# Kernel optimization log

Hardware: AMD Instinct MI355X
Metric: run time of the kernel (lower is better)

## Reference

```python
import jax, jax.numpy as jnp
import numpy as np

N = 100000      # active input voxels (== output voxels, stride=1)
K = 27          # kernel volume: 3**3 hypercube offsets
M = 50000       # active in/out pairs per kernel offset
CIN = 64
COUT = 64


def setup_inputs() -> dict:
    key = jax.random.key(0)
    k1, k2, k3, k4 = jax.random.split(key, 4)
    std = (2.0 / CIN / K) ** 0.5
    x = jax.random.normal(k1, (N, CIN), dtype=jnp.float32)
    kernel = jax.random.normal(k2, (K, CIN, COUT), dtype=jnp.float32) * std
    bias = jnp.zeros((1, COUT), dtype=jnp.float32)
    in_map = jax.random.randint(k3, (K, M), 0, N, dtype=jnp.int64)
    out_map = jax.random.randint(k4, (K, M), 0, N, dtype=jnp.int64)
    return {"x": x, "kernel": kernel, "bias": bias,
            "in_map": in_map, "out_map": out_map}


def reference(x, kernel, bias, in_map, out_map):
    # Sparse voxel convolution: per kernel-offset gather -> matmul -> scatter-add.
    gathered = x[in_map]                                   # [K, M, Cin]
    prod = jnp.einsum('kmc,kcd->kmd', gathered, kernel)    # [K, M, Cout]
    out = jnp.zeros((N, COUT), dtype=x.dtype)
    out = out.at[out_map.reshape(-1)].add(prod.reshape(-1, COUT))
    out = out + bias                                       # bias is [1, Cout]
    return out
```

## Files before the change

kernel.cpp:

```cpp
#include <hip/hip_runtime.h>
#include <hip/hip_fp16.h>

#define N_VOX 100000
#define KVOL 27
#define MPAIR 50000
#define CIN 64
#define COUT 64
#define TPW 4
#define NTILES 3125
#define GRIDX 196

typedef __attribute__((ext_vector_type(8))) short bf16x8;
typedef __attribute__((ext_vector_type(4))) float f32x4;
typedef __attribute__((ext_vector_type(4))) unsigned short u16x4;

__device__ inline unsigned short f2bf(float f) {
    union { float f; unsigned u; } v; v.f = f;
    return (unsigned short)((v.u + 0x7FFFu + ((v.u >> 16) & 1u)) >> 16);
}

__global__ void spconv_zero_ws(__half2* __restrict__ ws, int n2) {
    int i = blockIdx.x * blockDim.x + threadIdx.x;
    if (i < n2) ws[i] = __float2half2_rn(0.f);
}

__global__ void spconv_x_to_bf16(const float* __restrict__ x,
                                 unsigned short* __restrict__ xbf, int n4) {
    int i = blockIdx.x * blockDim.x + threadIdx.x;
    if (i >= n4) return;
    f32x4 v = ((const f32x4*)x)[i];
    u16x4 o; o.x = f2bf(v.x); o.y = f2bf(v.y); o.z = f2bf(v.z); o.w = f2bf(v.w);
    ((u16x4*)xbf)[i] = o;
}

__global__ void spconv_finalize(const __half2* __restrict__ ws,
                                const float* __restrict__ bias,
                                float* __restrict__ out, int n2) {
    int i = blockIdx.x * blockDim.x + threadIdx.x;
    if (i >= n2) return;
    float2 v = __half22float2(ws[i]);
    int c2 = (i & (COUT / 2 - 1)) * 2;
    float2 o; o.x = v.x + bias[c2]; o.y = v.y + bias[c2 + 1];
    ((float2*)out)[i] = o;
}

__global__ __launch_bounds__(256) void spconv_mlp_f16ws(
    const unsigned short* __restrict__ xbf,
    const float* __restrict__ kern,
    const int*   __restrict__ in_map,
    const int*   __restrict__ out_map,
    __half2*     __restrict__ ws)
{
    const int lane = threadIdx.x & 63;
    const int wave = threadIdx.x >> 6;
    const int k    = blockIdx.y;
    const int g    = lane >> 4;
    const int r16  = lane & 15;
    const int p    = r16 & 1;

    const int tile0 = (blockIdx.x * 4 + wave) * TPW;
    const int base0 = k * MPAIR;

    int inrow[TPW];
    #pragma unroll
    for (int t = 0; t < TPW; ++t) {
        int tl = tile0 + t; tl = tl < NTILES ? tl : NTILES - 1;
        inrow[t] = in_map[base0 + tl * 16 + r16];
    }

    bf16x8 afr[TPW][2];
    #pragma unroll
    for (int t = 0; t < TPW; ++t) {
        const unsigned short* xp = xbf + (size_t)inrow[t] * CIN + g * 8;
        afr[t][0] = *(const bf16x8*)(xp);
        afr[t][1] = *(const bf16x8*)(xp + 32);
    }

    int orow[TPW][4];
    #pragma unroll
    for (int t = 0; t < TPW; ++t) {
        int tl = tile0 + t; tl = tl < NTILES ? tl : NTILES - 1;
        #pragma unroll
        for (int r = 0; r < 4; ++r)
            orow[t][r] = out_map[base0 + tl * 16 + g * 4 + r];
    }

    bf16x8 bfrag[2][4];
    {
        const float* wp = kern + (size_t)k * CIN * COUT;
        #pragma unroll
        for (int s = 0; s < 2; ++s)
            #pragma unroll
            for (int q = 0; q < 4; ++q) {
                const float* pq = wp + (s * 32 + g * 8) * COUT + q * 16 + r16;
                bf16x8 f;
                #pragma unroll
                for (int j = 0; j < 8; ++j) f[j] = (short)f2bf(pq[j * COUT]);
                bfrag[s][q] = f;
            }
    }

    #pragma unroll
    for (int t = 0; t < TPW; ++t) {
        if (tile0 + t < NTILES) {
            f32x4 acc[4] = {{0.f,0.f,0.f,0.f},{0.f,0.f,0.f,0.f},
                            {0.f,0.f,0.f,0.f},{0.f,0.f,0.f,0.f}};
            #pragma unroll
            for (int q = 0; q < 4; ++q) {
                acc[q] = __builtin_amdgcn_mfma_f32_16x16x32_bf16(afr[t][0], bfrag[0][q], acc[q], 0, 0, 0);
                acc[q] = __builtin_amdgcn_mfma_f32_16x16x32_bf16(afr[t][1], bfrag[1][q], acc[q], 0, 0, 0);
            }
            #pragma unroll
            for (int r = 0; r < 4; ++r) {
                float pv[4];
                #pragma unroll
                for (int q = 0; q < 4; ++q) pv[q] = __shfl_xor(acc[q][r], 1);
                __half2* wrow = ws + (size_t)orow[t][r] * (COUT / 2);
                #pragma unroll
                for (int q = 0; q < 2; ++q) {
                    int tt = 2 * p + q;
                    float lo = p ? pv[tt] : acc[tt][r];
                    float hi = p ? acc[tt][r] : pv[tt];
                    int col = tt * 16 + r16 - p;
                    unsafeAtomicAdd(wrow + (col >> 1), __floats2half2_rn(lo, hi));
                }
            }
        }
    }
}

__global__ void spconv_init_bias(const float* __restrict__ bias,
                                 float* __restrict__ out, int total) {
    int i = blockIdx.x * blockDim.x + threadIdx.x;
    if (i < total) out[i] = bias[i & (COUT - 1)];
}

__global__ __launch_bounds__(256) void spconv_mfma_mlp(
    const unsigned short* __restrict__ xbf,
    const float* __restrict__ kern,
    const int*   __restrict__ in_map,
    const int*   __restrict__ out_map,
    float*       __restrict__ out)
{
    const int lane = threadIdx.x & 63;
    const int wave = threadIdx.x >> 6;
    const int k    = blockIdx.y;
    const int g    = lane >> 4;
    const int r16  = lane & 15;

    const int tile0 = (blockIdx.x * 4 + wave) * TPW;
    const int base0 = k * MPAIR;

    int inrow[TPW];
    #pragma unroll
    for (int t = 0; t < TPW; ++t) {
        int tl = tile0 + t; tl = tl < NTILES ? tl : NTILES - 1;
        inrow[t] = in_map[base0 + tl * 16 + r16];
    }
    bf16x8 afr[TPW][2];
    #pragma unroll
    for (int t = 0; t < TPW; ++t) {
        const unsigned short* xp = xbf + (size_t)inrow[t] * CIN + g * 8;
        afr[t][0] = *(const bf16x8*)(xp);
        afr[t][1] = *(const bf16x8*)(xp + 32);
    }
    int orow[TPW][4];
    #pragma unroll
    for (int t = 0; t < TPW; ++t) {
        int tl = tile0 + t; tl = tl < NTILES ? tl : NTILES - 1;
        #pragma unroll
        for (int r = 0; r < 4; ++r)
            orow[t][r] = out_map[base0 + tl * 16 + g * 4 + r];
    }
    bf16x8 bfrag[2][4];
    {
        const float* wp = kern + (size_t)k * CIN * COUT;
        #pragma unroll
        for (int s = 0; s < 2; ++s)
            #pragma unroll
            for (int q = 0; q < 4; ++q) {
                const float* pq = wp + (s * 32 + g * 8) * COUT + q * 16 + r16;
                bf16x8 f;
                #pragma unroll
                for (int j = 0; j < 8; ++j) f[j] = (short)f2bf(pq[j * COUT]);
                bfrag[s][q] = f;
            }
    }
    #pragma unroll
    for (int t = 0; t < TPW; ++t) {
        if (tile0 + t < NTILES) {
            f32x4 acc[4] = {{0.f,0.f,0.f,0.f},{0.f,0.f,0.f,0.f},
                            {0.f,0.f,0.f,0.f},{0.f,0.f,0.f,0.f}};
            #pragma unroll
            for (int q = 0; q < 4; ++q) {
                acc[q] = __builtin_amdgcn_mfma_f32_16x16x32_bf16(afr[t][0], bfrag[0][q], acc[q], 0, 0, 0);
                acc[q] = __builtin_amdgcn_mfma_f32_16x16x32_bf16(afr[t][1], bfrag[1][q], acc[q], 0, 0, 0);
            }
            #pragma unroll
            for (int r = 0; r < 4; ++r) {
                float* op = out + (size_t)orow[t][r] * COUT + r16;
                #pragma unroll
                for (int q = 0; q < 4; ++q)
                    atomicAdd(op + q * 16, acc[q][r]);
            }
        }
    }
}

extern "C" void kernel_launch(void* const* d_in, const int* in_sizes, int n_in,
                              void* d_out, int out_size, void* d_ws, size_t ws_size,
                              hipStream_t stream) {
    const float* x       = (const float*)d_in[0];
    const float* kern    = (const float*)d_in[1];
    const float* bias    = (const float*)d_in[2];
    const int*   in_map  = (const int*)d_in[3];
    const int*   out_map = (const int*)d_in[4];
    float*       out     = (float*)d_out;

    const size_t xbf_bytes = (size_t)N_VOX * CIN * sizeof(unsigned short);
    const size_t ws_bytes  = (size_t)N_VOX * COUT * sizeof(__half);
    int n4 = N_VOX * CIN / 4;
    int n2 = N_VOX * COUT / 2;
    dim3 grid(GRIDX, KVOL);

    if (ws_size >= xbf_bytes + ws_bytes) {
        unsigned short* xbf = (unsigned short*)d_ws;
        __half2* ws = (__half2*)((char*)d_ws + xbf_bytes);
        spconv_x_to_bf16<<<(n4 + 255) / 256, 256, 0, stream>>>(x, xbf, n4);
        spconv_zero_ws<<<(n2 + 255) / 256, 256, 0, stream>>>(ws, n2);
        spconv_mlp_f16ws<<<grid, 256, 0, stream>>>(xbf, kern, in_map, out_map, ws);
        spconv_finalize<<<(n2 + 255) / 256, 256, 0, stream>>>(ws, bias, out, n2);
    } else {
        unsigned short* xbf = (unsigned short*)d_ws;
        int total = N_VOX * COUT;
        spconv_init_bias<<<(total + 255) / 256, 256, 0, stream>>>(bias, out, total);
        spconv_x_to_bf16<<<(n4 + 255) / 256, 256, 0, stream>>>(x, xbf, n4);
        spconv_mfma_mlp<<<grid, 256, 0, stream>>>(xbf, kern, in_map, out_map, out);
    }
}
```

Measured before the change: 372.2 us.

## Replace atomic scatter-add with counting-sort slots and per-output segmented reduction

Removes the scatter-add atomics from the main kernel. A histogram over out_map assigns each pair a slot, and a single-block scan builds row pointers. The MFMA kernel then writes each product row as bf16 into its own slot with plain stores. A final kernel sums each output row's slots in fp32 and adds the bias. This trades about 43M half2 atomics for a much larger workspace and extra launches: histogram atomics, a serial single-block scan, and writing and reading back about 170MB of slots. The new path runs only when the workspace is big enough.

```diff
diff --git a/kernel.cpp b/kernel.cpp
--- a/kernel.cpp
+++ b/kernel.cpp
@@ -9,6 +9,7 @@
 #define TPW 4
 #define NTILES 3125
 #define GRIDX 196
+#define NPAIR (KVOL * MPAIR)
 
 typedef __attribute__((ext_vector_type(8))) short bf16x8;
 typedef __attribute__((ext_vector_type(4))) float f32x4;
@@ -18,11 +19,10 @@
     union { float f; unsigned u; } v; v.f = f;
     return (unsigned short)((v.u + 0x7FFFu + ((v.u >> 16) & 1u)) >> 16);
 }
-
-__global__ void spconv_zero_ws(__half2* __restrict__ ws, int n2) {
-    int i = blockIdx.x * blockDim.x + threadIdx.x;
-    if (i < n2) ws[i] = __float2half2_rn(0.f);
-}
+__device__ inline float bf2f(unsigned short u) {
+    union { unsigned u; float f; } v; v.u = (unsigned)u << 16; return v.f;
+}
+
 
 __global__ void spconv_x_to_bf16(const float* __restrict__ x,
                                  unsigned short* __restrict__ xbf, int n4) {
@@ -31,6 +31,147 @@
     f32x4 v = ((const f32x4*)x)[i];
     u16x4 o; o.x = f2bf(v.x); o.y = f2bf(v.y); o.z = f2bf(v.z); o.w = f2bf(v.w);
     ((u16x4*)xbf)[i] = o;
+}
+
+__global__ void spconv_zero_i32(int* __restrict__ p, int n) {
+    int i = blockIdx.x * blockDim.x + threadIdx.x;
+    if (i < n) p[i] = 0;
+}
+
+
+__global__ void spconv_hist_alloc(const int* __restrict__ out_map,
+                                  int* __restrict__ cnt,
+                                  int* __restrict__ off, int tot) {
+    int i = blockIdx.x * blockDim.x + threadIdx.x;
+    if (i < tot) off[i] = atomicAdd(&cnt[out_map[i]], 1);
+}
+
+__global__ __launch_bounds__(1024) void spconv_scan(const int* __restrict__ cnt,
+                                                    int* __restrict__ rowptr) {
+    __shared__ int part[1024];
+    const int T = 1024, C = (N_VOX + T - 1) / T;
+    int tid = threadIdx.x;
+    int base = tid * C, s = 0;
+    for (int j = 0; j < C; ++j) { int idx = base + j; if (idx < N_VOX) s += cnt[idx]; }
+    part[tid] = s;
+    __syncthreads();
+    for (int d = 1; d < T; d <<= 1) {
+        int v = (tid >= d) ? part[tid - d] : 0;
+        __syncthreads();
+        part[tid] += v;
+        __syncthreads();
+    }
+    int run = (tid == 0) ? 0 : part[tid - 1];
+    for (int j = 0; j < C; ++j) {
+        int idx = base + j;
+        if (idx < N_VOX) { rowptr[idx] = run; run += cnt[idx]; }
+    }
+    if (tid == T - 1) rowptr[N_VOX] = run;
+}
+
+__global__ __launch_bounds__(256) void spconv_phaseA(
+    const unsigned short* __restrict__ xbf,
+    const float* __restrict__ kern,
+    const int*   __restrict__ in_map,
+    const int*   __restrict__ out_map,
+    const int*   __restrict__ off,
+    const int*   __restrict__ rowptr,
+    unsigned short* __restrict__ slots)
+{
+    const int lane = threadIdx.x & 63;
+    const int wave = threadIdx.x >> 6;
+    const int k    = blockIdx.y;
+    const int g    = lane >> 4;
+    const int r16  = lane & 15;
+    const int p    = r16 & 1;
+
+    const int tile0 = (blockIdx.x * 4 + wave) * TPW;
+    const int base0 = k * MPAIR;
+
+    int inrow[TPW];
+    #pragma unroll
+    for (int t = 0; t < TPW; ++t) {
+        int tl = tile0 + t; tl = tl < NTILES ? tl : NTILES - 1;
+        inrow[t] = in_map[base0 + tl * 16 + r16];
+    }
+    bf16x8 afr[TPW][2];
+    #pragma unroll
+    for (int t = 0; t < TPW; ++t) {
+        const unsigned short* xp = xbf + (size_t)inrow[t] * CIN + g * 8;
+        afr[t][0] = *(const bf16x8*)(xp);
+        afr[t][1] = *(const bf16x8*)(xp + 32);
+    }
+    int sid_mine[TPW];
+    #pragma unroll
+    for (int t = 0; t < TPW; ++t) {
+        int tl = tile0 + t; tl = tl < NTILES ? tl : NTILES - 1;
+        int ip = base0 + tl * 16 + g * 4 + (r16 & 3);
+        sid_mine[t] = rowptr[out_map[ip]] + off[ip];
+    }
+    bf16x8 bfrag[2][4];
+    {
+        const float* wp = kern + (size_t)k * CIN * COUT;
+        #pragma unroll
+        for (int s = 0; s < 2; ++s)
+            #pragma unroll
+            for (int q = 0; q < 4; ++q) {
+                const float* pq = wp + (s * 32 + g * 8) * COUT + q * 16 + r16;
+                bf16x8 f;
+                #pragma unroll
+                for (int j = 0; j < 8; ++j) f[j] = (short)f2bf(pq[j * COUT]);
+                bfrag[s][q] = f;
+            }
+    }
+    #pragma unroll
+    for (int t = 0; t < TPW; ++t) {
+        if (tile0 + t < NTILES) {
+            f32x4 acc[4] = {{0.f,0.f,0.f,0.f},{0.f,0.f,0.f,0.f},
+                            {0.f,0.f,0.f,0.f},{0.f,0.f,0.f,0.f}};
+            #pragma unroll
+            for (int q = 0; q < 4; ++q) {
+                acc[q] = __builtin_amdgcn_mfma_f32_16x16x32_bf16(afr[t][0], bfrag[0][q], acc[q], 0, 0, 0);
+                acc[q] = __builtin_amdgcn_mfma_f32_16x16x32_bf16(afr[t][1], bfrag[1][q], acc[q], 0, 0, 0);
+            }
+            #pragma unroll
+            for (int r = 0; r < 4; ++r) {
+                int sid = __shfl(sid_mine[t], (lane & 48) + r);
+                float pv[4];
+                #pragma unroll
+                for (int q = 0; q < 4; ++q) pv[q] = __shfl_xor(acc[q][r], 1);
+                unsigned* srow = (unsigned*)(slots + (size_t)sid * COUT);
+                #pragma unroll
+                for (int q2 = 0; q2 < 2; ++q2) {
+                    int tt = 2 * p + q2;
+                    float lo = p ? pv[tt] : acc[tt][r];
+                    float hi = p ? acc[tt][r] : pv[tt];
+                    unsigned pk = (unsigned)f2bf(lo) | ((unsigned)f2bf(hi) << 16);
+                    int col = tt * 16 + r16 - p;
+                    srow[col >> 1] = pk;
+                }
+            }
+        }
+    }
+}
+
+__global__ __launch_bounds__(256) void spconv_phaseB(
+    const unsigned short* __restrict__ slots,
+    const int*   __restrict__ rowptr,
+    const float* __restrict__ bias,
+    float*       __restrict__ out)
+{
+    int w = threadIdx.x >> 6, l = threadIdx.x & 63;
+    int o = blockIdx.x * 4 + w;
+    int s0 = rowptr[o], s1 = rowptr[o + 1];
+    float acc = 0.f;
+    for (int s = s0; s < s1; ++s)
+        acc += bf2f(slots[(size_t)s * COUT + l]);
+    out[(size_t)o * COUT + l] = acc + bias[l];
+}
+
+
+__global__ void spconv_zero_ws(__half2* __restrict__ ws, int n2) {
+    int i = blockIdx.x * blockDim.x + threadIdx.x;
+    if (i < n2) ws[i] = __float2half2_rn(0.f);
 }
 
 __global__ void spconv_finalize(const __half2* __restrict__ ws,
@@ -67,7 +208,6 @@
         int tl = tile0 + t; tl = tl < NTILES ? tl : NTILES - 1;
         inrow[t] = in_map[base0 + tl * 16 + r16];
     }
-
     bf16x8 afr[TPW][2];
     #pragma unroll
     for (int t = 0; t < TPW; ++t) {
@@ -75,7 +215,6 @@
         afr[t][0] = *(const bf16x8*)(xp);
         afr[t][1] = *(const bf16x8*)(xp + 32);
     }
-
     int orow[TPW][4];
     #pragma unroll
     for (int t = 0; t < TPW; ++t) {
@@ -84,7 +223,6 @@
         for (int r = 0; r < 4; ++r)
             orow[t][r] = out_map[base0 + tl * 16 + g * 4 + r];
     }
-
     bf16x8 bfrag[2][4];
     {
         const float* wp = kern + (size_t)k * CIN * COUT;
@@ -99,7 +237,6 @@
                 bfrag[s][q] = f;
             }
     }
-
     #pragma unroll
     for (int t = 0; t < TPW; ++t) {
         if (tile0 + t < NTILES) {
@@ -117,8 +254,8 @@
                 for (int q = 0; q < 4; ++q) pv[q] = __shfl_xor(acc[q][r], 1);
                 __half2* wrow = ws + (size_t)orow[t][r] * (COUT / 2);
                 #pragma unroll
-                for (int q = 0; q < 2; ++q) {
-                    int tt = 2 * p + q;
+                for (int q2 = 0; q2 < 2; ++q2) {
+                    int tt = 2 * p + q2;
                     float lo = p ? pv[tt] : acc[tt][r];
                     float hi = p ? acc[tt][r] : pv[tt];
                     int col = tt * 16 + r16 - p;
@@ -129,83 +266,8 @@
     }
 }
 
-__global__ void spconv_init_bias(const float* __restrict__ bias,
-                                 float* __restrict__ out, int total) {
-    int i = blockIdx.x * blockDim.x + threadIdx.x;
-    if (i < total) out[i] = bias[i & (COUT - 1)];
-}
-
-__global__ __launch_bounds__(256) void spconv_mfma_mlp(
-    const unsigned short* __restrict__ xbf,
-    const float* __restrict__ kern,
-    const int*   __restrict__ in_map,
-    const int*   __restrict__ out_map,
-    float*       __restrict__ out)
-{
-    const int lane = threadIdx.x & 63;
-    const int wave = threadIdx.x >> 6;
-    const int k    = blockIdx.y;
-    const int g    = lane >> 4;
-    const int r16  = lane & 15;
-
-    const int tile0 = (blockIdx.x * 4 + wave) * TPW;
-    const int base0 = k * MPAIR;
-
-    int inrow[TPW];
-    #pragma unroll
-    for (int t = 0; t < TPW; ++t) {
-        int tl = tile0 + t; tl = tl < NTILES ? tl : NTILES - 1;
-        inrow[t] = in_map[base0 + tl * 16 + r16];
-    }
-    bf16x8 afr[TPW][2];
-    #pragma unroll
-    for (int t = 0; t < TPW; ++t) {
-        const unsigned short* xp = xbf + (size_t)inrow[t] * CIN + g * 8;
-        afr[t][0] = *(const bf16x8*)(xp);
-        afr[t][1] = *(const bf16x8*)(xp + 32);
-    }
-    int orow[TPW][4];
-    #pragma unroll
-    for (int t = 0; t < TPW; ++t) {
-        int tl = tile0 + t; tl = tl < NTILES ? tl : NTILES - 1;
-        #pragma unroll
-        for (int r = 0; r < 4; ++r)
-            orow[t][r] = out_map[base0 + tl * 16 + g * 4 + r];
-    }
-    bf16x8 bfrag[2][4];
-    {
-        const float* wp = kern + (size_t)k * CIN * COUT;
-        #pragma unroll
-        for (int s = 0; s < 2; ++s)
-            #pragma unroll
-            for (int q = 0; q < 4; ++q) {
-                const float* pq = wp + (s * 32 + g * 8) * COUT + q * 16 + r16;
-                bf16x8 f;
-                #pragma unroll
-                for (int j = 0; j < 8; ++j) f[j] = (short)f2bf(pq[j * COUT]);
-                bfrag[s][q] = f;
-            }
-    }
-    #pragma unroll
-    for (int t = 0; t < TPW; ++t) {
-        if (tile0 + t < NTILES) {
-            f32x4 acc[4] = {{0.f,0.f,0.f,0.f},{0.f,0.f,0.f,0.f},
-                            {0.f,0.f,0.f,0.f},{0.f,0.f,0.f,0.f}};
-            #pragma unroll
-            for (int q = 0; q < 4; ++q) {
-                acc[q] = __builtin_amdgcn_mfma_f32_16x16x32_bf16(afr[t][0], bfrag[0][q], acc[q], 0, 0, 0);
-                acc[q] = __builtin_amdgcn_mfma_f32_16x16x32_bf16(afr[t][1], bfrag[1][q], acc[q], 0, 0, 0);
-            }
-            #pragma unroll
-            for (int r = 0; r < 4; ++r) {
-                float* op = out + (size_t)orow[t][r] * COUT + r16;
-                #pragma unroll
-                for (int q = 0; q < 4; ++q)
-                    atomicAdd(op + q * 16, acc[q][r]);
-            }
-        }
-    }
-}
+
+static inline size_t al256(size_t a) { return (a + 255) & ~(size_t)255; }
 
 extern "C" void kernel_launch(void* const* d_in, const int* in_sizes, int n_in,
                               void* d_out, int out_size, void* d_ws, size_t ws_size,
@@ -217,24 +279,42 @@
     const int*   out_map = (const int*)d_in[4];
     float*       out     = (float*)d_out;
 
-    const size_t xbf_bytes = (size_t)N_VOX * CIN * sizeof(unsigned short);
-    const size_t ws_bytes  = (size_t)N_VOX * COUT * sizeof(__half);
+    const size_t xbf_b   = (size_t)N_VOX * CIN * 2;
+    const size_t cnt_b   = (size_t)(N_VOX + 1) * 4;
+    const size_t rp_b    = (size_t)(N_VOX + 1) * 4;
+    const size_t off_b   = (size_t)NPAIR * 4;
+    const size_t slots_b = (size_t)NPAIR * COUT * 2;
+
+    size_t o_xbf = 0;
+    size_t o_cnt = al256(o_xbf + xbf_b);
+    size_t o_rp  = al256(o_cnt + cnt_b);
+    size_t o_off = al256(o_rp + rp_b);
+    size_t o_sl  = al256(o_off + off_b);
+    size_t need  = o_sl + slots_b;
+
     int n4 = N_VOX * CIN / 4;
     int n2 = N_VOX * COUT / 2;
-    dim3 grid(GRIDX, KVOL);
-
-    if (ws_size >= xbf_bytes + ws_bytes) {
+    dim3 gridA(GRIDX, KVOL);
+
+    if (ws_size >= need) {
+        unsigned short* xbf   = (unsigned short*)((char*)d_ws + o_xbf);
+        int*            cnt   = (int*)((char*)d_ws + o_cnt);
+        int*            rowp  = (int*)((char*)d_ws + o_rp);
+        int*            off   = (int*)((char*)d_ws + o_off);
+        unsigned short* slots = (unsigned short*)((char*)d_ws + o_sl);
+
+        spconv_x_to_bf16<<<(n4 + 255) / 256, 256, 0, stream>>>(x, xbf, n4);
+        spconv_zero_i32<<<(N_VOX + 1 + 255) / 256, 256, 0, stream>>>(cnt, N_VOX + 1);
+        spconv_hist_alloc<<<(NPAIR + 255) / 256, 256, 0, stream>>>(out_map, cnt, off, NPAIR);
+        spconv_scan<<<1, 1024, 0, stream>>>(cnt, rowp);
+        spconv_phaseA<<<gridA, 256, 0, stream>>>(xbf, kern, in_map, out_map, off, rowp, slots);
+        spconv_phaseB<<<N_VOX / 4, 256, 0, stream>>>(slots, rowp, bias, out);
+    } else {
         unsigned short* xbf = (unsigned short*)d_ws;
-        __half2* ws = (__half2*)((char*)d_ws + xbf_bytes);
+        __half2* ws = (__half2*)((char*)d_ws + xbf_b);
         spconv_x_to_bf16<<<(n4 + 255) / 256, 256, 0, stream>>>(x, xbf, n4);
         spconv_zero_ws<<<(n2 + 255) / 256, 256, 0, stream>>>(ws, n2);
-        spconv_mlp_f16ws<<<grid, 256, 0, stream>>>(xbf, kern, in_map, out_map, ws);
+        spconv_mlp_f16ws<<<gridA, 256, 0, stream>>>(xbf, kern, in_map, out_map, ws);
         spconv_finalize<<<(n2 + 255) / 256, 256, 0, stream>>>(ws, bias, out, n2);
-    } else {
-        unsigned short* xbf = (unsigned short*)d_ws;
-        int total = N_VOX * COUT;
-        spconv_init_bias<<<(total + 255) / 256, 256, 0, stream>>>(bias, out, total);
-        spconv_x_to_bf16<<<(n4 + 255) / 256, 256, 0, stream>>>(x, xbf, n4);
-        spconv_mfma_mlp<<<grid, 256, 0, stream>>>(xbf, kern, in_map, out_map, out);
-    }
-}
+    }
+}
```

Result: slower. 482.9 us (+29.7%).
